# Kernel tuning notes

Measured on AMD Instinct MI355X. Metric: run time of the kernel, lower is better.

## Reference

```python
import jax, jax.numpy as jnp
import numpy as np
from jax import lax

DIM = 512          # model dim
L = 32             # img_size
N = L * L          # tokens
H = 4              # heads
C = DIM // 4       # channels per Res2Net scale
D = C // H         # per-head dim = 32 (== dim_head)
B = 8
SCALE = 32 ** -0.5  # dim_head ** -0.5
EPS = 1e-5


def setup_inputs() -> dict:
    key = jax.random.key(0)
    ks = jax.random.split(key, 13)
    nrm = lambda k, s, std: jax.random.normal(k, s, jnp.float32) * std
    uni = lambda k, s: jax.random.uniform(k, s, jnp.float32, 0.5, 1.5)
    return {
        "x": nrm(ks[0], (B, N, DIM), 1.0),
        "w_in": nrm(ks[1], (DIM, DIM), DIM ** -0.5),
        "bn1_g": uni(ks[2], (DIM,)),
        "bn1_b": nrm(ks[3], (DIM,), 0.1),
        "bn1_m": nrm(ks[4], (DIM,), 0.1),
        "bn1_v": uni(ks[5], (DIM,)),
        "w_dw": nrm(ks[6], (C, 1, 3, 3), 1.0 / 3.0),
        "w_pw": nrm(ks[7], (C, C), C ** -0.5),
        "bn2_g": uni(ks[8], (C,)),
        "bn2_b": nrm(ks[9], (C,), 0.1),
        "bn2_m": nrm(ks[10], (C,), 0.1),
        "bn2_v": uni(ks[11], (C,)),
        "w_out": nrm(ks[12], (DIM, DIM), DIM ** -0.5),
    }


def _bn(x, g, b, m, v):
    # eval-mode BatchNorm2d over NCHW
    inv = g / jnp.sqrt(v + EPS)
    return x * inv[None, :, None, None] + (b - m * inv)[None, :, None, None]


def _forward(x, w_in, bn1_g, bn1_b, bn1_m, bn1_v,
             w_dw, w_pw, bn2_g, bn2_b, bn2_m, bn2_v, w_out):
    b = x.shape[0]
    # 'b (l w) n -> b n l w'
    xi = x.transpose(0, 2, 1).reshape(b, DIM, L, L)
    # Res2Net: inconv (1x1 conv + BN)
    ident = jnp.einsum('oc,bchw->bohw', w_in, xi)
    ident = _bn(ident, bn1_g, bn1_b, bn1_m, bn1_v)
    xs = jnp.split(ident, 4, axis=1)

    def x3conv(t):
        t = lax.conv_general_dilated(
            t, w_dw, window_strides=(1, 1), padding='SAME',
            feature_group_count=C,
            dimension_numbers=('NCHW', 'OIHW', 'NCHW'))
        t = jnp.einsum('oc,bchw->bohw', w_pw, t)
        return _bn(t, bn2_g, bn2_b, bn2_m, bn2_v)

    ys = [xs[0]]
    ys.append(x3conv(xs[1]))
    ys.append(x3conv(xs[2] + ys[1]))
    ys.append(x3conv(xs[3] + ys[2]))
    y = jnp.stack(ys, axis=1)  # [b, 4, C, L, L]

    # 'b (h d) l w -> b h (l w) d' per scale; batch the 4 scales together
    qkv = y.reshape(b, 4, H, D, N).transpose(0, 1, 2, 4, 3)  # [b,4,h,n,d]
    att = jnp.einsum('bshid,bshjd->bshij', qkv, qkv) * SCALE   # [b,4,h,n,n]
    att = jax.nn.softmax(att, axis=-1)
    o = jnp.einsum('bshij,bshjd->bshid', att, qkv)             # [b,4,h,n,d]
    # cat over scales of 'b h n d -> b n (h d)' => [b, n, (s h d)] = [b, n, DIM]
    o = o.transpose(0, 3, 1, 2, 4).reshape(b, N, DIM)
    return o @ w_out.T  # Linear(dim, dim, bias=False); dropout is identity (eval)


def reference(x, w_in, bn1_g, bn1_b, bn1_m, bn1_v,
              w_dw, w_pw, bn2_g, bn2_b, bn2_m, bn2_v, w_out):
    return _forward(x, w_in, bn1_g, bn1_b, bn1_m, bn1_v,
                    w_dw, w_pw, bn2_g, bn2_b, bn2_m, bn2_v, w_out)
```

## Files before the change

kernel.cpp:

```cpp
#include <hip/hip_runtime.h>
#include <hip/hip_bf16.h>


#define DIMM 512
#define NTOK 1024
#define CC   128
#define DD   32
#define BB   8
#define EPSB 1e-5f
#define SCALE_ATT 0.17677669529663687f
#define K2EXP (SCALE_ATT * 1.4426950408889634f)
#define TJ 128

typedef __attribute__((ext_vector_type(8))) short short8;
typedef __attribute__((ext_vector_type(4))) float f32x4;

__device__ __forceinline__ unsigned short f2bf(float f) {
    unsigned int x = __float_as_uint(f);
    unsigned int r = x + 0x7fffu + ((x >> 16) & 1u);
    return (unsigned short)(r >> 16);
}
__device__ __forceinline__ unsigned int f2bf2(float lo, float hi) {
    return (unsigned int)f2bf(lo) | ((unsigned int)f2bf(hi) << 16);
}

__global__ __launch_bounds__(256) void k_mm_in(
    const float* __restrict__ w_in,
    const float* __restrict__ x,
    const float* __restrict__ g1, const float* __restrict__ b1,
    const float* __restrict__ m1, const float* __restrict__ v1,
    float* __restrict__ Y)
{
    __shared__ __align__(16) unsigned short As[128][72];
    __shared__ __align__(16) unsigned short Bs[128][72];
    const int r0 = blockIdx.x * 128;
    const int o0 = blockIdx.y * 128;
    const int b  = r0 >> 10, nloc0 = r0 & 1023;
    const int t = threadIdx.x, wid = t >> 6, lane = t & 63;
    const int l16 = lane & 15, quad = lane >> 4;
    const int wm = (wid >> 1) * 64, wn = (wid & 1) * 64;

    f32x4 acc[4][4];
#pragma unroll
    for (int i = 0; i < 4; i++)
#pragma unroll
        for (int j = 0; j < 4; j++) acc[i][j] = (f32x4){0.f, 0.f, 0.f, 0.f};

    for (int k0 = 0; k0 < DIMM; k0 += 64) {
        __syncthreads();
#pragma unroll
        for (int it = 0; it < 8; it++) {
            int flat = it * 256 + t;
            int row = flat >> 4, c4 = flat & 15;
            float4 w4 = *(const float4*)&w_in[(size_t)(o0 + row) * DIMM + k0 + c4 * 4];
            *(uint2*)&As[row][c4 * 4] = make_uint2(f2bf2(w4.x, w4.y), f2bf2(w4.z, w4.w));
            float4 x4 = *(const float4*)&x[(size_t)(r0 + row) * DIMM + k0 + c4 * 4];
            *(uint2*)&Bs[row][c4 * 4] = make_uint2(f2bf2(x4.x, x4.y), f2bf2(x4.z, x4.w));
        }
        __syncthreads();
#pragma unroll
        for (int kk = 0; kk < 2; kk++) {
            short8 af[4], bf_[4];
#pragma unroll
            for (int i = 0; i < 4; i++) af[i]  = *(const short8*)&As[wm + i * 16 + l16][kk * 32 + quad * 8];
#pragma unroll
            for (int j = 0; j < 4; j++) bf_[j] = *(const short8*)&Bs[wn + j * 16 + l16][kk * 32 + quad * 8];
#pragma unroll
            for (int i = 0; i < 4; i++)
#pragma unroll
                for (int j = 0; j < 4; j++)
                    acc[i][j] = __builtin_amdgcn_mfma_f32_16x16x32_bf16(af[i], bf_[j], acc[i][j], 0, 0, 0);
        }
    }
#pragma unroll
    for (int i = 0; i < 4; i++)
#pragma unroll
        for (int r = 0; r < 4; r++) {
            int o = o0 + wm + i * 16 + quad * 4 + r;
            float inv  = g1[o] / sqrtf(v1[o] + EPSB);
            float beta = b1[o] - m1[o] * inv;
#pragma unroll
            for (int j = 0; j < 4; j++) {
                int n = nloc0 + wn + j * 16 + l16;
                Y[((size_t)b * DIMM + o) * NTOK + n] = acc[i][j][r] * inv + beta;
            }
        }
}

__global__ __launch_bounds__(256) void k_dwconv(
    const float* __restrict__ Y, const float* __restrict__ w_dw,
    float* __restrict__ tmp, int s)
{
    __shared__ float img[34][34];
    const int c = blockIdx.x;
    const int b = blockIdx.y;
    const int t = threadIdx.x;
    for (int i = t; i < 34 * 34; i += 256) (&img[0][0])[i] = 0.f;
    __syncthreads();
    const float* src0 = Y + ((size_t)b * DIMM + s * CC + c) * NTOK;
    const float* src1 = (s >= 2) ? (Y + ((size_t)b * DIMM + (s - 1) * CC + c) * NTOK) : nullptr;
    for (int p = t; p < NTOK; p += 256) {
        float v = src0[p];
        if (src1) v += src1[p];
        img[(p >> 5) + 1][(p & 31) + 1] = v;
    }
    __syncthreads();
    float w[9];
#pragma unroll
    for (int i = 0; i < 9; i++) w[i] = w_dw[c * 9 + i];
    for (int p = t; p < NTOK; p += 256) {
        int yy = p >> 5, xx = p & 31;
        float s0 = 0.f;
#pragma unroll
        for (int ky = 0; ky < 3; ky++)
#pragma unroll
            for (int kx = 0; kx < 3; kx++)
                s0 += img[yy + ky][xx + kx] * w[ky * 3 + kx];
        tmp[((size_t)b * CC + c) * NTOK + p] = s0;
    }
}

__global__ __launch_bounds__(256) void k_mm_pw(
    const float* __restrict__ tmp, const float* __restrict__ w_pw,
    const float* __restrict__ g2, const float* __restrict__ b2,
    const float* __restrict__ m2, const float* __restrict__ v2,
    float* __restrict__ Y, int s)
{
    __shared__ __align__(16) unsigned short As[128][72];
    __shared__ __align__(16) unsigned short Bs[64][72];
    const int n0 = blockIdx.x * 64;
    const int b  = blockIdx.y;
    const int t = threadIdx.x, wid = t >> 6, lane = t & 63;
    const int l16 = lane & 15, quad = lane >> 4;
    const int wm = (wid >> 1) * 64, wn = (wid & 1) * 32;

    f32x4 acc[4][2];
#pragma unroll
    for (int i = 0; i < 4; i++) { acc[i][0] = (f32x4){0.f,0.f,0.f,0.f}; acc[i][1] = (f32x4){0.f,0.f,0.f,0.f}; }

    for (int k0 = 0; k0 < CC; k0 += 64) {
        __syncthreads();
#pragma unroll
        for (int it = 0; it < 8; it++) {
            int flat = it * 256 + t;
            int row = flat >> 4, c4 = flat & 15;
            float4 w4 = *(const float4*)&w_pw[(size_t)row * CC + k0 + c4 * 4];
            *(uint2*)&As[row][c4 * 4] = make_uint2(f2bf2(w4.x, w4.y), f2bf2(w4.z, w4.w));
        }
#pragma unroll
        for (int it = 0; it < 4; it++) {
            int flat = it * 256 + t;
            int c = flat >> 4, n4 = (flat & 15) * 4;
            float4 v = *(const float4*)&tmp[((size_t)b * CC + k0 + c) * NTOK + n0 + n4];
            Bs[n4 + 0][c] = f2bf(v.x);
            Bs[n4 + 1][c] = f2bf(v.y);
            Bs[n4 + 2][c] = f2bf(v.z);
            Bs[n4 + 3][c] = f2bf(v.w);
        }
        __syncthreads();
#pragma unroll
        for (int kk = 0; kk < 2; kk++) {
            short8 af[4], bf_[2];
#pragma unroll
            for (int i = 0; i < 4; i++) af[i]  = *(const short8*)&As[wm + i * 16 + l16][kk * 32 + quad * 8];
#pragma unroll
            for (int j = 0; j < 2; j++) bf_[j] = *(const short8*)&Bs[wn + j * 16 + l16][kk * 32 + quad * 8];
#pragma unroll
            for (int i = 0; i < 4; i++)
#pragma unroll
                for (int j = 0; j < 2; j++)
                    acc[i][j] = __builtin_amdgcn_mfma_f32_16x16x32_bf16(af[i], bf_[j], acc[i][j], 0, 0, 0);
        }
    }
#pragma unroll
    for (int i = 0; i < 4; i++)
#pragma unroll
        for (int r = 0; r < 4; r++) {
            int o = wm + i * 16 + quad * 4 + r;
            float inv  = g2[o] / sqrtf(v2[o] + EPSB);
            float beta = b2[o] - m2[o] * inv;
#pragma unroll
            for (int j = 0; j < 2; j++) {
                int n = n0 + wn + j * 16 + l16;
                Y[((size_t)b * DIMM + s * CC + o) * NTOK + n] = acc[i][j][r] * inv + beta;
            }
        }
}

__global__ __launch_bounds__(256) void k_prep(
    const float* __restrict__ Y,
    unsigned short* __restrict__ Vp,
    unsigned short* __restrict__ Qt)
{
    __shared__ float T[32][129];
    const int jt = blockIdx.x;
    const int n0 = jt * 128;
    const int g  = blockIdx.y;
    const int b = g >> 4, s = (g >> 2) & 3, h = g & 3;
    const int cb = s * CC + h * DD;
    const int t = threadIdx.x;
#pragma unroll
    for (int k = 0; k < 8; k++) {
        int idx = k * 256 + t;
        int d = idx >> 6, jp = (idx & 63) * 2;
        float2 v = *(const float2*)&Y[((size_t)b * DIMM + cb + d) * NTOK + n0 + jp];
        T[d][jp] = v.x; T[d][jp + 1] = v.y;
    }
    __syncthreads();
#pragma unroll
    for (int k = 0; k < 8; k++) {
        int idx = k * 256 + t;
        int n = idx >> 4, dp = (idx & 15) * 2;
        *(unsigned int*)&Qt[((size_t)g * NTOK + n0 + n) * DD + dp] = f2bf2(T[dp][n], T[dp + 1][n]);
    }
#pragma unroll
    for (int e2 = 0; e2 < 2; e2++) {
        int e = e2 * 256 + t;
        int sub = e >> 6, lane = e & 63;
        int quad = lane >> 4, l16 = lane & 15;
        int d  = (sub & 1) * 16 + l16;
        int jb = (sub >> 1) * 32 + quad * 4;
        uint4 v;
        v.x = f2bf2(T[d][jb + 0],  T[d][jb + 1]);
        v.y = f2bf2(T[d][jb + 2],  T[d][jb + 3]);
        v.z = f2bf2(T[d][jb + 16], T[d][jb + 17]);
        v.w = f2bf2(T[d][jb + 18], T[d][jb + 19]);
        *(uint4*)&Vp[((((size_t)g * 8 + jt) * 8 + sub) * 64 + lane) * 8] = v;
    }
}

__global__ __launch_bounds__(256) void k_attn(
    const unsigned short* __restrict__ Qtg,
    const unsigned short* __restrict__ Vp,
    unsigned short* __restrict__ Ob)
{
    const int blk = blockIdx.x;
    const int g = blk & 127, ib = blk >> 7;
    const int b = g >> 4, s = (g >> 2) & 3, h = g & 3;
    const int cb = s * CC + h * DD;
    const unsigned short* Qt = Qtg + (size_t)g * NTOK * DD;
    const unsigned short* Vg = Vp + (size_t)g * 8 * 8 * 64 * 8;
    const int t = threadIdx.x;
    const int wid = t >> 6, lane = t & 63;
    const int l16 = lane & 15, quad = lane >> 4;
    const int i = ib * 64 + wid * 16 + l16;

    const short8 qi = *(const short8*)&Qt[(size_t)i * DD + quad * 8];
    const short8 ones = {0x3F80, 0x3F80, 0x3F80, 0x3F80, 0x3F80, 0x3F80, 0x3F80, 0x3F80};

    float m_run = -INFINITY;
    f32x4 lacc = {0.f, 0.f, 0.f, 0.f};
    f32x4 oacc[2] = {{0.f,0.f,0.f,0.f},{0.f,0.f,0.f,0.f}};
    const f32x4 zero4 = {0.f, 0.f, 0.f, 0.f};

#pragma unroll 2
    for (int jt = 0; jt < 8; jt++) {
        const int j0 = jt * TJ;
        f32x4 sacc[8];
#pragma unroll
        for (int jb = 0; jb < 8; jb++) {
            short8 qj = *(const short8*)&Qt[(size_t)(j0 + jb * 16 + l16) * DD + quad * 8];
            sacc[jb] = __builtin_amdgcn_mfma_f32_16x16x32_bf16(qj, qi, zero4, 0, 0, 0);
        }
        float mx = fmaxf(fmaxf(sacc[0][0], sacc[0][1]), fmaxf(sacc[0][2], sacc[0][3]));
#pragma unroll
        for (int jb = 1; jb < 8; jb++) {
            float m2_ = fmaxf(fmaxf(sacc[jb][0], sacc[jb][1]), fmaxf(sacc[jb][2], sacc[jb][3]));
            mx = fmaxf(mx, m2_);
        }
        mx = fmaxf(mx, __shfl_xor(mx, 16));
        mx = fmaxf(mx, __shfl_xor(mx, 32));

        float mn = fmaxf(m_run, mx);
        float al = exp2f((m_run - mn) * K2EXP);
        m_run = mn;
        float mnk = mn * K2EXP;

        short8 pb[4];
#pragma unroll
        for (int jb = 0; jb < 8; jb++) {
            float p0 = exp2f(fmaf(sacc[jb][0], K2EXP, -mnk));
            float p1 = exp2f(fmaf(sacc[jb][1], K2EXP, -mnk));
            float p2 = exp2f(fmaf(sacc[jb][2], K2EXP, -mnk));
            float p3 = exp2f(fmaf(sacc[jb][3], K2EXP, -mnk));
            ((unsigned int*)&pb[jb >> 1])[(jb & 1) * 2]     =
                __builtin_amdgcn_perm(__float_as_uint(p1), __float_as_uint(p0), 0x07060302u);
            ((unsigned int*)&pb[jb >> 1])[(jb & 1) * 2 + 1] =
                __builtin_amdgcn_perm(__float_as_uint(p3), __float_as_uint(p2), 0x07060302u);
        }

#pragma unroll
        for (int r = 0; r < 4; r++) { oacc[0][r] *= al; oacc[1][r] *= al; lacc[r] *= al; }

#pragma unroll
        for (int wp = 0; wp < 4; wp++) {
            short8 af0 = *(const short8*)&Vg[(((size_t)jt * 8 + wp * 2 + 0) * 64 + lane) * 8];
            short8 af1 = *(const short8*)&Vg[(((size_t)jt * 8 + wp * 2 + 1) * 64 + lane) * 8];
            oacc[0] = __builtin_amdgcn_mfma_f32_16x16x32_bf16(af0, pb[wp], oacc[0], 0, 0, 0);
            oacc[1] = __builtin_amdgcn_mfma_f32_16x16x32_bf16(af1, pb[wp], oacc[1], 0, 0, 0);
            lacc    = __builtin_amdgcn_mfma_f32_16x16x32_bf16(ones, pb[wp], lacc, 0, 0, 0);
        }
    }

    float invl = 1.f / lacc[0];
#pragma unroll
    for (int dblk = 0; dblk < 2; dblk++) {
        uint2 pkd;
        pkd.x = f2bf2(oacc[dblk][0] * invl, oacc[dblk][1] * invl);
        pkd.y = f2bf2(oacc[dblk][2] * invl, oacc[dblk][3] * invl);
        *(uint2*)&Ob[((size_t)b * NTOK + i) * DIMM + cb + dblk * 16 + quad * 4] = pkd;
    }
}

__global__ __launch_bounds__(256) void k_mm_out(
    const unsigned short* __restrict__ Oin,
    const float* __restrict__ w_out,
    float* __restrict__ out)
{
    __shared__ __align__(16) unsigned short As[128][72];
    __shared__ __align__(16) unsigned short Bs[128][72];
    const int r0 = blockIdx.x * 128;
    const int o0 = blockIdx.y * 128;
    const int t = threadIdx.x, wid = t >> 6, lane = t & 63;
    const int l16 = lane & 15, quad = lane >> 4;
    const int wm = (wid >> 1) * 64, wn = (wid & 1) * 64;

    f32x4 acc[4][4];
#pragma unroll
    for (int i = 0; i < 4; i++)
#pragma unroll
        for (int j = 0; j < 4; j++) acc[i][j] = (f32x4){0.f, 0.f, 0.f, 0.f};

    for (int k0 = 0; k0 < DIMM; k0 += 64) {
        __syncthreads();
#pragma unroll
        for (int q = 0; q < 4; q++) {
            int flat = q * 256 + t;
            int row = flat >> 3, c8 = flat & 7;
            *(short8*)&As[row][c8 * 8] = *(const short8*)&Oin[(size_t)(r0 + row) * DIMM + k0 + c8 * 8];
        }
#pragma unroll
        for (int it = 0; it < 8; it++) {
            int flat = it * 256 + t;
            int row = flat >> 4, c4 = flat & 15;
            float4 w4 = *(const float4*)&w_out[(size_t)(o0 + row) * DIMM + k0 + c4 * 4];
            *(uint2*)&Bs[row][c4 * 4] = make_uint2(f2bf2(w4.x, w4.y), f2bf2(w4.z, w4.w));
        }
        __syncthreads();
#pragma unroll
        for (int kk = 0; kk < 2; kk++) {
            short8 af[4], bf_[4];
#pragma unroll
            for (int i = 0; i < 4; i++) af[i]  = *(const short8*)&As[wm + i * 16 + l16][kk * 32 + quad * 8];
#pragma unroll
            for (int j = 0; j < 4; j++) bf_[j] = *(const short8*)&Bs[wn + j * 16 + l16][kk * 32 + quad * 8];
#pragma unroll
            for (int i = 0; i < 4; i++)
#pragma unroll
                for (int j = 0; j < 4; j++)
                    acc[i][j] = __builtin_amdgcn_mfma_f32_16x16x32_bf16(af[i], bf_[j], acc[i][j], 0, 0, 0);
        }
    }
#pragma unroll
    for (int i = 0; i < 4; i++)
#pragma unroll
        for (int r = 0; r < 4; r++) {
            int rr = r0 + wm + i * 16 + quad * 4 + r;
#pragma unroll
            for (int j = 0; j < 4; j++) {
                int o = o0 + wn + j * 16 + l16;
                out[(size_t)rr * DIMM + o] = acc[i][j][r];
            }
        }
}

extern "C" void kernel_launch(void* const* d_in, const int* in_sizes, int n_in,
                              void* d_out, int out_size, void* d_ws, size_t ws_size,
                              hipStream_t stream)
{
    const float* x    = (const float*)d_in[0];
    const float* w_in = (const float*)d_in[1];
    const float* g1   = (const float*)d_in[2];
    const float* b1   = (const float*)d_in[3];
    const float* m1   = (const float*)d_in[4];
    const float* v1   = (const float*)d_in[5];
    const float* wdw  = (const float*)d_in[6];
    const float* wpw  = (const float*)d_in[7];
    const float* g2   = (const float*)d_in[8];
    const float* b2   = (const float*)d_in[9];
    const float* m2   = (const float*)d_in[10];
    const float* v2   = (const float*)d_in[11];
    const float* wout = (const float*)d_in[12];
    float* out = (float*)d_out;

    char* base = (char*)d_ws;
    float*          Y   = (float*)base;
    unsigned short* Ob  = (unsigned short*)base;
    float*          tmp = (float*)(base + (size_t)16 * 1024 * 1024);
    unsigned short* Vp  = (unsigned short*)(base + (size_t)16 * 1024 * 1024);
    unsigned short* Qt  = (unsigned short*)(base + (size_t)24 * 1024 * 1024);

    k_mm_in<<<dim3(64, 4), 256, 0, stream>>>(w_in, x, g1, b1, m1, v1, Y);
    for (int s = 1; s <= 3; s++) {
        k_dwconv<<<dim3(CC, BB), 256, 0, stream>>>(Y, wdw, tmp, s);
        k_mm_pw<<<dim3(16, 8), 256, 0, stream>>>(tmp, wpw, g2, b2, m2, v2, Y, s);
    }
    k_prep<<<dim3(8, 128), 256, 0, stream>>>(Y, Vp, Qt);
    k_attn<<<dim3(2048), 256, 0, stream>>>(Qt, Vp, Ob);
    k_mm_out<<<dim3(64, 4), 256, 0, stream>>>(Ob, wout, out);
}
```

Baseline: 228.3 us.

## Pre-convert inputs to bf16 and shrink GEMM tiles for more blocks

Adds a conversion kernel that turns x, w_in and w_pw into bf16 up front, so the input GEMM and pointwise GEMM load bf16 directly instead of converting inside their tile loops. The input, pointwise and output GEMMs now use smaller output tiles and launch more blocks, which should fill the device better: the pointwise GEMM goes from 128 to 256 blocks and the others double as well. The cost is an extra launch plus an extra full pass over x (read fp32, write bf16), and operand tiles get re-read more often.

Result: slower. 241.5 us (+5.8%).

```diff
diff --git a/kernel.cpp b/kernel.cpp
--- a/kernel.cpp
+++ b/kernel.cpp
@@ -24,51 +24,71 @@
     return (unsigned int)f2bf(lo) | ((unsigned int)f2bf(hi) << 16);
 }
 
+#define CVT_NX (BB * NTOK * DIMM)
+#define CVT_NW (DIMM * DIMM)
+#define CVT_NP (CC * CC)
+#define CVT_TOT4 ((CVT_NX + CVT_NW + CVT_NP) / 4)
+__global__ __launch_bounds__(256) void k_cvt4(
+    const float* __restrict__ x, const float* __restrict__ wi, const float* __restrict__ wp,
+    unsigned short* __restrict__ xb, unsigned short* __restrict__ wib, unsigned short* __restrict__ wpwb)
+{
+    int idx = blockIdx.x * 256 + threadIdx.x;
+    if (idx >= CVT_TOT4) return;
+    int e = idx * 4;
+    const float* src; unsigned short* dst; int off;
+    if (e < CVT_NX)                 { src = x;  dst = xb;   off = e; }
+    else if (e < CVT_NX + CVT_NW)   { src = wi; dst = wib;  off = e - CVT_NX; }
+    else                            { src = wp; dst = wpwb; off = e - CVT_NX - CVT_NW; }
+    float4 v = *(const float4*)&src[off];
+    *(uint2*)&dst[off] = make_uint2(f2bf2(v.x, v.y), f2bf2(v.z, v.w));
+}
+
 __global__ __launch_bounds__(256) void k_mm_in(
-    const float* __restrict__ w_in,
-    const float* __restrict__ x,
+    const unsigned short* __restrict__ Wb,
+    const unsigned short* __restrict__ Xb,
     const float* __restrict__ g1, const float* __restrict__ b1,
     const float* __restrict__ m1, const float* __restrict__ v1,
     float* __restrict__ Y)
 {
     __shared__ __align__(16) unsigned short As[128][72];
-    __shared__ __align__(16) unsigned short Bs[128][72];
-    const int r0 = blockIdx.x * 128;
+    __shared__ __align__(16) unsigned short Bs[64][72];
+    const int r0 = blockIdx.x * 64;
     const int o0 = blockIdx.y * 128;
     const int b  = r0 >> 10, nloc0 = r0 & 1023;
     const int t = threadIdx.x, wid = t >> 6, lane = t & 63;
     const int l16 = lane & 15, quad = lane >> 4;
-    const int wm = (wid >> 1) * 64, wn = (wid & 1) * 64;
-
-    f32x4 acc[4][4];
-#pragma unroll
-    for (int i = 0; i < 4; i++)
-#pragma unroll
-        for (int j = 0; j < 4; j++) acc[i][j] = (f32x4){0.f, 0.f, 0.f, 0.f};
+    const int wm = (wid >> 1) * 64, wn = (wid & 1) * 32;
+
+    f32x4 acc[4][2];
+#pragma unroll
+    for (int i = 0; i < 4; i++) { acc[i][0] = (f32x4){0.f,0.f,0.f,0.f}; acc[i][1] = (f32x4){0.f,0.f,0.f,0.f}; }
 
     for (int k0 = 0; k0 < DIMM; k0 += 64) {
         __syncthreads();
 #pragma unroll
-        for (int it = 0; it < 8; it++) {
-            int flat = it * 256 + t;
-            int row = flat >> 4, c4 = flat & 15;
-            float4 w4 = *(const float4*)&w_in[(size_t)(o0 + row) * DIMM + k0 + c4 * 4];
-            *(uint2*)&As[row][c4 * 4] = make_uint2(f2bf2(w4.x, w4.y), f2bf2(w4.z, w4.w));
-            float4 x4 = *(const float4*)&x[(size_t)(r0 + row) * DIMM + k0 + c4 * 4];
-            *(uint2*)&Bs[row][c4 * 4] = make_uint2(f2bf2(x4.x, x4.y), f2bf2(x4.z, x4.w));
+        for (int it = 0; it < 4; it++) {
+            int flat = it * 256 + t;
+            int row = flat >> 3, c8 = flat & 7;
+            *(short8*)&As[row][c8 * 8] = *(const short8*)&Wb[(size_t)(o0 + row) * DIMM + k0 + c8 * 8];
+        }
+#pragma unroll
+        for (int it = 0; it < 2; it++) {
+            int flat = it * 256 + t;
+            int row = flat >> 3, c8 = flat & 7;
+            *(short8*)&Bs[row][c8 * 8] = *(const short8*)&Xb[(size_t)(r0 + row) * DIMM + k0 + c8 * 8];
         }
         __syncthreads();
 #pragma unroll
         for (int kk = 0; kk < 2; kk++) {
-            short8 af[4], bf_[4];
+            short8 af[4], bf_[2];
 #pragma unroll
             for (int i = 0; i < 4; i++) af[i]  = *(const short8*)&As[wm + i * 16 + l16][kk * 32 + quad * 8];
 #pragma unroll
-            for (int j = 0; j < 4; j++) bf_[j] = *(const short8*)&Bs[wn + j * 16 + l16][kk * 32 + quad * 8];
+            for (int j = 0; j < 2; j++) bf_[j] = *(const short8*)&Bs[wn + j * 16 + l16][kk * 32 + quad * 8];
 #pragma unroll
             for (int i = 0; i < 4; i++)
 #pragma unroll
-                for (int j = 0; j < 4; j++)
+                for (int j = 0; j < 2; j++)
                     acc[i][j] = __builtin_amdgcn_mfma_f32_16x16x32_bf16(af[i], bf_[j], acc[i][j], 0, 0, 0);
         }
     }
@@ -80,7 +100,7 @@
             float inv  = g1[o] / sqrtf(v1[o] + EPSB);
             float beta = b1[o] - m1[o] * inv;
 #pragma unroll
-            for (int j = 0; j < 4; j++) {
+            for (int j = 0; j < 2; j++) {
                 int n = nloc0 + wn + j * 16 + l16;
                 Y[((size_t)b * DIMM + o) * NTOK + n] = acc[i][j][r] * inv + beta;
             }
@@ -121,31 +141,31 @@
 }
 
 __global__ __launch_bounds__(256) void k_mm_pw(
-    const float* __restrict__ tmp, const float* __restrict__ w_pw,
+    const float* __restrict__ tmp, const unsigned short* __restrict__ Wpwb,
     const float* __restrict__ g2, const float* __restrict__ b2,
     const float* __restrict__ m2, const float* __restrict__ v2,
     float* __restrict__ Y, int s)
 {
-    __shared__ __align__(16) unsigned short As[128][72];
+    __shared__ __align__(16) unsigned short As[64][72];
     __shared__ __align__(16) unsigned short Bs[64][72];
     const int n0 = blockIdx.x * 64;
-    const int b  = blockIdx.y;
+    const int o0 = blockIdx.y * 64;
+    const int b  = blockIdx.z;
     const int t = threadIdx.x, wid = t >> 6, lane = t & 63;
     const int l16 = lane & 15, quad = lane >> 4;
-    const int wm = (wid >> 1) * 64, wn = (wid & 1) * 32;
-
-    f32x4 acc[4][2];
-#pragma unroll
-    for (int i = 0; i < 4; i++) { acc[i][0] = (f32x4){0.f,0.f,0.f,0.f}; acc[i][1] = (f32x4){0.f,0.f,0.f,0.f}; }
+    const int wm = (wid >> 1) * 32, wn = (wid & 1) * 32;
+
+    f32x4 acc[2][2];
+#pragma unroll
+    for (int i = 0; i < 2; i++) { acc[i][0] = (f32x4){0.f,0.f,0.f,0.f}; acc[i][1] = (f32x4){0.f,0.f,0.f,0.f}; }
 
     for (int k0 = 0; k0 < CC; k0 += 64) {
         __syncthreads();
 #pragma unroll
-        for (int it = 0; it < 8; it++) {
-            int flat = it * 256 + t;
-            int row = flat >> 4, c4 = flat & 15;
-            float4 w4 = *(const float4*)&w_pw[(size_t)row * CC + k0 + c4 * 4];
-            *(uint2*)&As[row][c4 * 4] = make_uint2(f2bf2(w4.x, w4.y), f2bf2(w4.z, w4.w));
+        for (int it = 0; it < 2; it++) {
+            int flat = it * 256 + t;
+            int row = flat >> 3, c8 = flat & 7;
+            *(short8*)&As[row][c8 * 8] = *(const short8*)&Wpwb[(size_t)(o0 + row) * CC + k0 + c8 * 8];
         }
 #pragma unroll
         for (int it = 0; it < 4; it++) {
@@ -160,23 +180,23 @@
         __syncthreads();
 #pragma unroll
         for (int kk = 0; kk < 2; kk++) {
-            short8 af[4], bf_[2];
-#pragma unroll
-            for (int i = 0; i < 4; i++) af[i]  = *(const short8*)&As[wm + i * 16 + l16][kk * 32 + quad * 8];
+            short8 af[2], bf_[2];
+#pragma unroll
+            for (int i = 0; i < 2; i++) af[i]  = *(const short8*)&As[wm + i * 16 + l16][kk * 32 + quad * 8];
 #pragma unroll
             for (int j = 0; j < 2; j++) bf_[j] = *(const short8*)&Bs[wn + j * 16 + l16][kk * 32 + quad * 8];
 #pragma unroll
-            for (int i = 0; i < 4; i++)
+            for (int i = 0; i < 2; i++)
 #pragma unroll
                 for (int j = 0; j < 2; j++)
                     acc[i][j] = __builtin_amdgcn_mfma_f32_16x16x32_bf16(af[i], bf_[j], acc[i][j], 0, 0, 0);
         }
     }
 #pragma unroll
-    for (int i = 0; i < 4; i++)
+    for (int i = 0; i < 2; i++)
 #pragma unroll
         for (int r = 0; r < 4; r++) {
-            int o = wm + i * 16 + quad * 4 + r;
+            int o = o0 + wm + i * 16 + quad * 4 + r;
             float inv  = g2[o] / sqrtf(v2[o] + EPSB);
             float beta = b2[o] - m2[o] * inv;
 #pragma unroll
@@ -318,29 +338,27 @@
     float* __restrict__ out)
 {
     __shared__ __align__(16) unsigned short As[128][72];
-    __shared__ __align__(16) unsigned short Bs[128][72];
+    __shared__ __align__(16) unsigned short Bs[64][72];
     const int r0 = blockIdx.x * 128;
-    const int o0 = blockIdx.y * 128;
+    const int o0 = blockIdx.y * 64;
     const int t = threadIdx.x, wid = t >> 6, lane = t & 63;
     const int l16 = lane & 15, quad = lane >> 4;
-    const int wm = (wid >> 1) * 64, wn = (wid & 1) * 64;
-
-    f32x4 acc[4][4];
-#pragma unroll
-    for (int i = 0; i < 4; i++)
-#pragma unroll
-        for (int j = 0; j < 4; j++) acc[i][j] = (f32x4){0.f, 0.f, 0.f, 0.f};
+    const int wm = (wid >> 1) * 64, wn = (wid & 1) * 32;
+
+    f32x4 acc[4][2];
+#pragma unroll
+    for (int i = 0; i < 4; i++) { acc[i][0] = (f32x4){0.f,0.f,0.f,0.f}; acc[i][1] = (f32x4){0.f,0.f,0.f,0.f}; }
 
     for (int k0 = 0; k0 < DIMM; k0 += 64) {
         __syncthreads();
 #pragma unroll
-        for (int q = 0; q < 4; q++) {
-            int flat = q * 256 + t;
+        for (int it = 0; it < 4; it++) {
+            int flat = it * 256 + t;
             int row = flat >> 3, c8 = flat & 7;
             *(short8*)&As[row][c8 * 8] = *(const short8*)&Oin[(size_t)(r0 + row) * DIMM + k0 + c8 * 8];
         }
 #pragma unroll
-        for (int it = 0; it < 8; it++) {
+        for (int it = 0; it < 4; it++) {
             int flat = it * 256 + t;
             int row = flat >> 4, c4 = flat & 15;
             float4 w4 = *(const float4*)&w_out[(size_t)(o0 + row) * DIMM + k0 + c4 * 4];
@@ -349,15 +367,15 @@
         __syncthreads();
 #pragma unroll
         for (int kk = 0; kk < 2; kk++) {
-            short8 af[4], bf_[4];
+            short8 af[4], bf_[2];
 #pragma unroll
             for (int i = 0; i < 4; i++) af[i]  = *(const short8*)&As[wm + i * 16 + l16][kk * 32 + quad * 8];
 #pragma unroll
-            for (int j = 0; j < 4; j++) bf_[j] = *(const short8*)&Bs[wn + j * 16 + l16][kk * 32 + quad * 8];
+            for (int j = 0; j < 2; j++) bf_[j] = *(const short8*)&Bs[wn + j * 16 + l16][kk * 32 + quad * 8];
 #pragma unroll
             for (int i = 0; i < 4; i++)
 #pragma unroll
-                for (int j = 0; j < 4; j++)
+                for (int j = 0; j < 2; j++)
                     acc[i][j] = __builtin_amdgcn_mfma_f32_16x16x32_bf16(af[i], bf_[j], acc[i][j], 0, 0, 0);
         }
     }
@@ -367,7 +385,7 @@
         for (int r = 0; r < 4; r++) {
             int rr = r0 + wm + i * 16 + quad * 4 + r;
 #pragma unroll
-            for (int j = 0; j < 4; j++) {
+            for (int j = 0; j < 2; j++) {
                 int o = o0 + wn + j * 16 + l16;
                 out[(size_t)rr * DIMM + o] = acc[i][j][r];
             }
@@ -394,18 +412,22 @@
     float* out = (float*)d_out;
 
     char* base = (char*)d_ws;
-    float*          Y   = (float*)base;
-    unsigned short* Ob  = (unsigned short*)base;
-    float*          tmp = (float*)(base + (size_t)16 * 1024 * 1024);
-    unsigned short* Vp  = (unsigned short*)(base + (size_t)16 * 1024 * 1024);
-    unsigned short* Qt  = (unsigned short*)(base + (size_t)24 * 1024 * 1024);
-
-    k_mm_in<<<dim3(64, 4), 256, 0, stream>>>(w_in, x, g1, b1, m1, v1, Y);
+    float*          Y    = (float*)base;
+    unsigned short* Ob   = (unsigned short*)base;
+    unsigned short* xb   = (unsigned short*)(base + (size_t)16 * 1024 * 1024);
+    float*          tmp  = (float*)(base + (size_t)16 * 1024 * 1024);
+    unsigned short* Vp   = (unsigned short*)(base + (size_t)16 * 1024 * 1024);
+    unsigned short* wib  = (unsigned short*)(base + (size_t)24 * 1024 * 1024);
+    unsigned short* wpwb = (unsigned short*)(base + (size_t)24 * 1024 * 1024 + 524288);
+    unsigned short* Qt   = (unsigned short*)(base + (size_t)24 * 1024 * 1024);
+
+    k_cvt4<<<dim3((CVT_TOT4 + 255) / 256), 256, 0, stream>>>(x, w_in, wpw, xb, wib, wpwb);
+    k_mm_in<<<dim3(128, 4), 256, 0, stream>>>(wib, xb, g1, b1, m1, v1, Y);
     for (int s = 1; s <= 3; s++) {
         k_dwconv<<<dim3(CC, BB), 256, 0, stream>>>(Y, wdw, tmp, s);
-        k_mm_pw<<<dim3(16, 8), 256, 0, stream>>>(tmp, wpw, g2, b2, m2, v2, Y, s);
+        k_mm_pw<<<dim3(16, 2, 8), 256, 0, stream>>>(tmp, wpwb, g2, b2, m2, v2, Y, s);
     }
     k_prep<<<dim3(8, 128), 256, 0, stream>>>(Y, Vp, Qt);
     k_attn<<<dim3(2048), 256, 0, stream>>>(Qt, Vp, Ob);
-    k_mm_out<<<dim3(64, 4), 256, 0, stream>>>(Ob, wout, out);
-}
+    k_mm_out<<<dim3(64, 8), 256, 0, stream>>>(Ob, wout, out);
+}
```
